# Optimization experiments

Hardware: AMD Instinct MI355X
Metric: run time of the kernel (lower is better)

## Reference

```python
import jax, jax.numpy as jnp
import numpy as np

B = 16384      # batch of protein embeddings
C = 128        # n_channels
F = 5000       # number of GO terms (functions)
E_CHILD = 15000  # parent->child edges (~3 children per term)


def setup_inputs() -> dict:
    key = jax.random.key(0)
    k_x, k_w, k_p, k_c = jax.random.split(key, 4)
    x = jax.random.normal(k_x, (B, C), dtype=jnp.float32)
    W = jax.random.normal(k_w, (C, F), dtype=jnp.float32) * 0.05
    b = jnp.zeros((F,), dtype=jnp.float32)
    # random GO DAG edges; every node also gets a self-edge so the max
    # aggregation covers {self} U children, exactly like the torch loop
    parents = jax.random.randint(k_p, (E_CHILD,), 0, F, dtype=jnp.int32)
    childs = jax.random.randint(k_c, (E_CHILD,), 0, F, dtype=jnp.int32)
    self_idx = jnp.arange(F, dtype=jnp.int32)
    edge_parent = jnp.concatenate([self_idx, parents])  # [20000]
    edge_child = jnp.concatenate([self_idx, childs])    # [20000]
    return {"x": x, "W": W, "b": b,
            "edge_parent": edge_parent, "edge_child": edge_child}


def reference(x, W, b, edge_parent, edge_child):
    # Fused version of the 5000 separate Linear(C,1)+Sigmoid heads
    probs = jax.nn.sigmoid(x @ W + b)          # [B, F]
    # Hierarchical max over {self} U children via segment-max on edge list
    vals = probs.T[edge_child]                  # [E, B]
    agg = jax.ops.segment_max(vals, edge_parent, num_segments=F)  # [F, B]
    return agg.T                                # [B, F]
```

## Files before the change

kernel.cpp:

```cpp
#include <hip/hip_runtime.h>
#include <hip/hip_bf16.h>

#define BDIM 16384
#define CDIM 128
#define FDIM 5000
#define EDIM 20000
#define ELLW 16
#define MAXOVF 20000
#define NT4  10

typedef __attribute__((ext_vector_type(8))) short short8;
typedef __attribute__((ext_vector_type(4))) float f32x4;
typedef __attribute__((ext_vector_type(2))) float f32x2;
typedef __attribute__((ext_vector_type(2))) int i32x2;
typedef __attribute__((ext_vector_type(8))) unsigned short upk8;
typedef __attribute__((ext_vector_type(4))) unsigned short upk4;
typedef __attribute__((ext_vector_type(2))) unsigned int u32x2;

__device__ __forceinline__ unsigned short f2bf(float f) {
    unsigned int u = __builtin_bit_cast(unsigned int, f);
    u = (u + 0x7fffu + ((u >> 16) & 1u)) >> 16;
    return (unsigned short)u;
}
__device__ __forceinline__ float bf2f(unsigned short s) {
    unsigned int u = ((unsigned int)s) << 16;
    return __builtin_bit_cast(float, u);
}
__device__ __forceinline__ unsigned short q2bf(unsigned int w, int k) {
    float f = (float)((w >> (8 * k)) & 0xFFu);
    return (unsigned short)(__builtin_bit_cast(unsigned int, f) >> 16);
}
__device__ __forceinline__ upk8 umax8(upk8 a, upk8 b) {
#if __has_builtin(__builtin_elementwise_max)
    return __builtin_elementwise_max(a, b);
#else
    upk8 r;
    #pragma unroll
    for (int j = 0; j < 8; ++j) r[j] = a[j] > b[j] ? a[j] : b[j];
    return r;
#endif
}
__device__ __forceinline__ float fast_rcp(float x) {
#if __has_builtin(__builtin_amdgcn_rcpf)
    return __builtin_amdgcn_rcpf(x);
#else
    return 1.0f / x;
#endif
}
__device__ __forceinline__ void gll16(const unsigned short* g, unsigned short* l) {
    __builtin_amdgcn_global_load_lds(
        (const __attribute__((address_space(1))) void*)g,
        (__attribute__((address_space(3))) void*)l, 16, 0, 0);
}

__global__ __launch_bounds__(256) void prep1_kernel(
    const float* __restrict__ x, const float* __restrict__ W,
    unsigned short* __restrict__ xb, unsigned short* __restrict__ wt,
    unsigned short* __restrict__ ell, int* __restrict__ cur,
    int* __restrict__ ovf_cnt)
{
    __shared__ float lt[128][33];
    int bid = blockIdx.x, tid = threadIdx.x;
    if (bid < 1024) {
        size_t base = (size_t)bid * 2048 + (size_t)tid * 8;
        const f32x4* p = (const f32x4*)(x + base);
        f32x4 v0 = p[0], v1 = p[1];
        short8 o;
        o[0] = (short)f2bf(v0[0]); o[1] = (short)f2bf(v0[1]);
        o[2] = (short)f2bf(v0[2]); o[3] = (short)f2bf(v0[3]);
        o[4] = (short)f2bf(v1[0]); o[5] = (short)f2bf(v1[1]);
        o[6] = (short)f2bf(v1[2]); o[7] = (short)f2bf(v1[3]);
        *(short8*)(xb + base) = o;
    } else if (bid < 1181) {
        int f0 = (bid - 1024) * 32;
        int f_l = tid & 31, k0 = (tid >> 5) * 16;
        #pragma unroll
        for (int i = 0; i < 16; ++i) {
            int f = f0 + f_l;
            lt[k0 + i][f_l] = (f < FDIM) ? W[(size_t)(k0 + i) * FDIM + f] : 0.f;
        }
        __syncthreads();
        int f_l2 = tid >> 3, ks = (tid & 7) * 16;
        int f = f0 + f_l2;
        if (f < FDIM) {
            short8 o0, o1;
            #pragma unroll
            for (int j = 0; j < 8; ++j) o0[j] = (short)f2bf(lt[ks + j][f_l2]);
            #pragma unroll
            for (int j = 0; j < 8; ++j) o1[j] = (short)f2bf(lt[ks + 8 + j][f_l2]);
            *(short8*)(wt + (size_t)f * 128 + ks)     = o0;
            *(short8*)(wt + (size_t)f * 128 + ks + 8) = o1;
        }
    } else {
        int p = (bid - 1181) * 256 + tid;
        if (p < FDIM) {
            upk8 s;
            #pragma unroll
            for (int j = 0; j < 8; ++j) s[j] = (unsigned short)p;
            *(upk8*)(ell + (size_t)p * ELLW)     = s;
            *(upk8*)(ell + (size_t)p * ELLW + 8) = s;
            cur[p] = 1;
        }
        if (p == FDIM) *ovf_cnt = 0;
    }
}

__global__ __launch_bounds__(256) void prep2_kernel(
    const int* __restrict__ epar, const int* __restrict__ echild,
    int* __restrict__ cur, unsigned short* __restrict__ ell,
    int* __restrict__ ovf_cnt, int* __restrict__ ovf_pairs)
{
    int i = blockIdx.x * 256 + threadIdx.x;
    if (i < EDIM) {
        int p = epar[i], c = echild[i];
        if (p != c) {
            int pos = atomicAdd(&cur[p], 1);
            if (pos < ELLW) {
                ell[(size_t)p * ELLW + pos] = (unsigned short)c;
            } else {
                int j = atomicAdd(ovf_cnt, 1);
                if (j < MAXOVF) { ovf_pairs[2 * j] = p; ovf_pairs[2 * j + 1] = c; }
            }
        }
    }
}

__global__ __launch_bounds__(512, 4) void gemm8i4_kernel(
    const unsigned short* __restrict__ xb,
    const unsigned short* __restrict__ wt,
    const float* __restrict__ bias,
    unsigned char* __restrict__ probs8)
{
    __shared__ unsigned short lA[128 * 128];
    __shared__ unsigned short lB[128 * 128];

    int bid0 = blockIdx.x;
    int bid  = (bid0 & 7) * (128 * NT4 / 8) + (bid0 >> 3);
    int bm = bid / NT4, bq = bid % NT4;
    int tid = threadIdx.x;
    int lane = tid & 63, w = tid >> 6;
    int wm = w >> 2, wn = w & 3;
    int g = lane >> 4, lr = lane & 15;
    int lrow = lane >> 4;
    int lcol = (lane & 15) << 4;

    auto stageA = [&]() {
        #pragma unroll
        for (int it = 0; it < 4; ++it) {
            int ci = w * 4 + it;
            int row = ci * 4 + lrow;
            int sw = lcol ^ ((row & 7) << 4);
            gll16(xb + ((size_t)(bm * 128 + row) << 7) + (sw >> 1),
                  lA + ci * 512);
        }
    };
    auto stageB = [&](int bn) {
        #pragma unroll
        for (int it = 0; it < 4; ++it) {
            int ci = w * 4 + it;
            int row = ci * 4 + lrow;
            int sw = lcol ^ ((row & 7) << 4);
            gll16(wt + ((size_t)(bn * 128 + row) << 7) + (sw >> 1),
                  lB + ci * 512);
        }
    };
    auto compute = [&](f32x4 (&acc)[4][2]) {
        #pragma unroll
        for (int ks = 0; ks < 4; ++ks) {
            int cbk = ks * 64 + g * 16;
            short8 af[4], bf[2];
            #pragma unroll
            for (int mi = 0; mi < 4; ++mi) {
                int row = wm * 64 + mi * 16 + lr;
                af[mi] = *(const short8*)((const char*)lA + row * 256 + (cbk ^ ((row & 7) << 4)));
            }
            #pragma unroll
            for (int nj = 0; nj < 2; ++nj) {
                int row = wn * 32 + nj * 16 + lr;
                bf[nj] = *(const short8*)((const char*)lB + row * 256 + (cbk ^ ((row & 7) << 4)));
            }
            #pragma unroll
            for (int mi = 0; mi < 4; ++mi)
                #pragma unroll
                for (int nj = 0; nj < 2; ++nj)
                    acc[mi][nj] = __builtin_amdgcn_mfma_f32_16x16x32_bf16(
                        af[mi], bf[nj], acc[mi][nj], 0, 0, 0);
        }
    };
    auto epilogue = [&](int bn, f32x4 (&acc)[4][2]) {
        #pragma unroll
        for (int nj = 0; nj < 2; ++nj) {
            int f = bn * 128 + wn * 32 + nj * 16 + lr;
            bool ok = (f < FDIM);
            float bb = ok ? bias[f] : 0.f;
            #pragma unroll
            for (int mi = 0; mi < 4; ++mi) {
                unsigned int pk = 0;
                #pragma unroll
                for (int j = 0; j < 4; ++j) {
                    float z = acc[mi][nj][j] + bb;
                    float pr = fast_rcp(1.0f + __expf(-z));
                    unsigned int q = (unsigned int)(pr * 255.f + 0.5f);
                    pk |= q << (8 * j);
                }
                if (ok) {
                    int slab = bm * 16 + wm * 8 + mi * 2 + (g >> 1);
                    *(unsigned int*)(probs8 + ((size_t)slab * FDIM + f) * 8 + (g & 1) * 4) = pk;
                }
            }
        }
    };

    stageA();
    stageB(bq * 4);
    __syncthreads();

    f32x4 zero = {0.f, 0.f, 0.f, 0.f};
    for (int t = 0; t < 4; ++t) {
        f32x4 acc[4][2];
        #pragma unroll
        for (int mi = 0; mi < 4; ++mi) { acc[mi][0] = zero; acc[mi][1] = zero; }
        compute(acc);
        if (t < 3) {
            __syncthreads();
            stageB(bq * 4 + t + 1);
            epilogue(bq * 4 + t, acc);
            __syncthreads();
        } else {
            epilogue(bq * 4 + t, acc);
        }
    }
}

__global__ __launch_bounds__(1024) void segmax10_kernel(
    const unsigned char* __restrict__ probs8,
    const int* __restrict__ cur, const unsigned short* __restrict__ ell,
    const int* __restrict__ ovf_cnt, const int* __restrict__ ovf_pairs,
    float* __restrict__ out)
{
    __shared__ unsigned short l[FDIM * 8];
    int slab = blockIdx.x;
    int b0 = slab * 8;
    int tid = threadIdx.x;
    const unsigned char* src = probs8 + (size_t)slab * FDIM * 8;

    for (int c = tid; c < FDIM; c += 1024) {
        u32x2 v = *(const u32x2*)(src + (size_t)c * 8);
        upk8 o;
        #pragma unroll
        for (int k = 0; k < 4; ++k) {
            o[k]     = q2bf(v[0], k);
            o[4 + k] = q2bf(v[1], k);
        }
        *(upk8*)(l + (size_t)c * 8) = o;
    }
    __syncthreads();

    int novf = *ovf_cnt; if (novf > MAXOVF) novf = MAXOVF;

    for (int p0 = tid * 2; p0 < FDIM; p0 += 2048) {
        int p1 = p0 + 1;
        i32x2 dg = *(const i32x2*)(cur + p0);
        upk4 ea = *(const upk4*)(ell + (size_t)p0 * ELLW);
        upk4 eb = *(const upk4*)(ell + (size_t)p1 * ELLW);
        upk8 ma = *(const upk8*)(l + (size_t)ea[0] * 8);
        upk8 mb = *(const upk8*)(l + (size_t)eb[0] * 8);
        ma = umax8(ma, *(const upk8*)(l + (size_t)ea[1] * 8));
        mb = umax8(mb, *(const upk8*)(l + (size_t)eb[1] * 8));
        ma = umax8(ma, *(const upk8*)(l + (size_t)ea[2] * 8));
        mb = umax8(mb, *(const upk8*)(l + (size_t)eb[2] * 8));
        ma = umax8(ma, *(const upk8*)(l + (size_t)ea[3] * 8));
        mb = umax8(mb, *(const upk8*)(l + (size_t)eb[3] * 8));
        if (dg[0] > 4) {
            upk4 e = *(const upk4*)(ell + (size_t)p0 * ELLW + 4);
            ma = umax8(ma, *(const upk8*)(l + (size_t)e[0] * 8));
            ma = umax8(ma, *(const upk8*)(l + (size_t)e[1] * 8));
            ma = umax8(ma, *(const upk8*)(l + (size_t)e[2] * 8));
            ma = umax8(ma, *(const upk8*)(l + (size_t)e[3] * 8));
        }
        if (dg[1] > 4) {
            upk4 e = *(const upk4*)(ell + (size_t)p1 * ELLW + 4);
            mb = umax8(mb, *(const upk8*)(l + (size_t)e[0] * 8));
            mb = umax8(mb, *(const upk8*)(l + (size_t)e[1] * 8));
            mb = umax8(mb, *(const upk8*)(l + (size_t)e[2] * 8));
            mb = umax8(mb, *(const upk8*)(l + (size_t)e[3] * 8));
        }
        if (dg[0] > 8) {
            upk8 e = *(const upk8*)(ell + (size_t)p0 * ELLW + 8);
            #pragma unroll
            for (int j = 0; j < 8; ++j)
                ma = umax8(ma, *(const upk8*)(l + (size_t)e[j] * 8));
        }
        if (dg[1] > 8) {
            upk8 e = *(const upk8*)(ell + (size_t)p1 * ELLW + 8);
            #pragma unroll
            for (int j = 0; j < 8; ++j)
                mb = umax8(mb, *(const upk8*)(l + (size_t)e[j] * 8));
        }
        if (dg[0] > ELLW) {
            for (int i = 0; i < novf; ++i)
                if (ovf_pairs[2 * i] == p0)
                    ma = umax8(ma, *(const upk8*)(l + (size_t)ovf_pairs[2 * i + 1] * 8));
        }
        if (dg[1] > ELLW) {
            for (int i = 0; i < novf; ++i)
                if (ovf_pairs[2 * i] == p1)
                    mb = umax8(mb, *(const upk8*)(l + (size_t)ovf_pairs[2 * i + 1] * 8));
        }
        size_t o = (size_t)b0 * FDIM + p0;
        #pragma unroll
        for (int r = 0; r < 8; ++r) {
            f32x2 v2;
            v2[0] = bf2f(ma[r]) * (1.f / 255.f);
            v2[1] = bf2f(mb[r]) * (1.f / 255.f);
            __builtin_nontemporal_store(v2, (f32x2*)(out + o + (size_t)r * FDIM));
        }
    }
}

extern "C" void kernel_launch(void* const* d_in, const int* in_sizes, int n_in,
                              void* d_out, int out_size, void* d_ws, size_t ws_size,
                              hipStream_t stream)
{
    const float* x     = (const float*)d_in[0];
    const float* W     = (const float*)d_in[1];
    const float* bias  = (const float*)d_in[2];
    const int*   epar  = (const int*)d_in[3];
    const int*   echild= (const int*)d_in[4];
    float* out = (float*)d_out;

    char* ws = (char*)d_ws;
    size_t off = 0;
    auto alloc = [&](size_t bytes) { size_t o = off; off = (off + bytes + 255) & ~(size_t)255; return o; };
    size_t o_probs  = alloc((size_t)BDIM * FDIM);
    size_t o_xb     = alloc((size_t)BDIM * CDIM * 2);
    size_t o_wt     = alloc((size_t)FDIM * CDIM * 2);
    size_t o_ell    = alloc((size_t)FDIM * ELLW * 2);
    size_t o_cur    = alloc((size_t)FDIM * 4);
    size_t o_ovfc   = alloc(4);
    size_t o_ovfp   = alloc((size_t)MAXOVF * 8);
    (void)ws_size; (void)in_sizes; (void)n_in; (void)out_size;

    unsigned char*  probs8 = (unsigned char*)(ws + o_probs);
    unsigned short* xb     = (unsigned short*)(ws + o_xb);
    unsigned short* wt     = (unsigned short*)(ws + o_wt);
    unsigned short* ell    = (unsigned short*)(ws + o_ell);
    int* cur      = (int*)(ws + o_cur);
    int* ovf_cnt  = (int*)(ws + o_ovfc);
    int* ovf_pairs= (int*)(ws + o_ovfp);

    prep1_kernel<<<1201, 256, 0, stream>>>(x, W, xb, wt, ell, cur, ovf_cnt);
    prep2_kernel<<<79, 256, 0, stream>>>(epar, echild, cur, ell, ovf_cnt, ovf_pairs);
    gemm8i4_kernel<<<128 * NT4, 512, 0, stream>>>(xb, wt, bias, probs8);
    segmax10_kernel<<<BDIM / 8, 1024, 0, stream>>>(probs8, cur, ell,
                                                   ovf_cnt, ovf_pairs, out);
}
```

Before: 159.2 us.

## Fuse GEMM and segment-max into persistent kernel with dynamic task queue

Result: slower. 220.6 us (+38.5%).

```diff
diff --git a/kernel.cpp b/kernel.cpp
--- a/kernel.cpp
+++ b/kernel.cpp
@@ -8,6 +8,10 @@
 #define ELLW 16
 #define MAXOVF 20000
 #define NT4  10
+#define NGEMM 1280
+#define NSEG  2048
+#define NBM   128
+#define LAGB  52
 
 typedef __attribute__((ext_vector_type(8))) short short8;
 typedef __attribute__((ext_vector_type(4))) float f32x4;
@@ -57,7 +61,8 @@
     const float* __restrict__ x, const float* __restrict__ W,
     unsigned short* __restrict__ xb, unsigned short* __restrict__ wt,
     unsigned short* __restrict__ ell, int* __restrict__ cur,
-    int* __restrict__ ovf_cnt)
+    int* __restrict__ ovf_cnt, int* __restrict__ task_ctr,
+    int* __restrict__ bm_done)
 {
     __shared__ float lt[128][33];
     int bid = blockIdx.x, tid = threadIdx.x;
@@ -101,7 +106,8 @@
             *(upk8*)(ell + (size_t)p * ELLW + 8) = s;
             cur[p] = 1;
         }
-        if (p == FDIM) *ovf_cnt = 0;
+        if (p < NBM) bm_done[p] = 0;
+        if (p == FDIM) { *ovf_cnt = 0; *task_ctr = 0; }
     }
 }
 
@@ -125,196 +131,229 @@
     }
 }
 
-__global__ __launch_bounds__(512, 4) void gemm8i4_kernel(
+__global__ __launch_bounds__(512, 4) void fused_kernel(
     const unsigned short* __restrict__ xb,
     const unsigned short* __restrict__ wt,
     const float* __restrict__ bias,
-    unsigned char* __restrict__ probs8)
+    unsigned char* __restrict__ probs8,
+    const int* __restrict__ cur, const unsigned short* __restrict__ ell,
+    const int* __restrict__ ovf_cnt, const int* __restrict__ ovf_pairs,
+    float* __restrict__ out,
+    int* __restrict__ task_ctr, int* __restrict__ bm_done)
 {
-    __shared__ unsigned short lA[128 * 128];
-    __shared__ unsigned short lB[128 * 128];
-
-    int bid0 = blockIdx.x;
-    int bid  = (bid0 & 7) * (128 * NT4 / 8) + (bid0 >> 3);
-    int bm = bid / NT4, bq = bid % NT4;
+    __shared__ unsigned short smem[40000];
+    __shared__ int sTask;
+
     int tid = threadIdx.x;
     int lane = tid & 63, w = tid >> 6;
     int wm = w >> 2, wn = w & 3;
     int g = lane >> 4, lr = lane & 15;
     int lrow = lane >> 4;
     int lcol = (lane & 15) << 4;
-
-    auto stageA = [&]() {
-        #pragma unroll
-        for (int it = 0; it < 4; ++it) {
-            int ci = w * 4 + it;
-            int row = ci * 4 + lrow;
-            int sw = lcol ^ ((row & 7) << 4);
-            gll16(xb + ((size_t)(bm * 128 + row) << 7) + (sw >> 1),
-                  lA + ci * 512);
-        }
-    };
-    auto stageB = [&](int bn) {
-        #pragma unroll
-        for (int it = 0; it < 4; ++it) {
-            int ci = w * 4 + it;
-            int row = ci * 4 + lrow;
-            int sw = lcol ^ ((row & 7) << 4);
-            gll16(wt + ((size_t)(bn * 128 + row) << 7) + (sw >> 1),
-                  lB + ci * 512);
-        }
-    };
-    auto compute = [&](f32x4 (&acc)[4][2]) {
-        #pragma unroll
-        for (int ks = 0; ks < 4; ++ks) {
-            int cbk = ks * 64 + g * 16;
-            short8 af[4], bf[2];
-            #pragma unroll
-            for (int mi = 0; mi < 4; ++mi) {
-                int row = wm * 64 + mi * 16 + lr;
-                af[mi] = *(const short8*)((const char*)lA + row * 256 + (cbk ^ ((row & 7) << 4)));
-            }
-            #pragma unroll
-            for (int nj = 0; nj < 2; ++nj) {
-                int row = wn * 32 + nj * 16 + lr;
-                bf[nj] = *(const short8*)((const char*)lB + row * 256 + (cbk ^ ((row & 7) << 4)));
-            }
-            #pragma unroll
-            for (int mi = 0; mi < 4; ++mi)
-                #pragma unroll
-                for (int nj = 0; nj < 2; ++nj)
-                    acc[mi][nj] = __builtin_amdgcn_mfma_f32_16x16x32_bf16(
-                        af[mi], bf[nj], acc[mi][nj], 0, 0, 0);
-        }
-    };
-    auto epilogue = [&](int bn, f32x4 (&acc)[4][2]) {
-        #pragma unroll
-        for (int nj = 0; nj < 2; ++nj) {
-            int f = bn * 128 + wn * 32 + nj * 16 + lr;
-            bool ok = (f < FDIM);
-            float bb = ok ? bias[f] : 0.f;
-            #pragma unroll
-            for (int mi = 0; mi < 4; ++mi) {
-                unsigned int pk = 0;
-                #pragma unroll
-                for (int j = 0; j < 4; ++j) {
-                    float z = acc[mi][nj][j] + bb;
-                    float pr = fast_rcp(1.0f + __expf(-z));
-                    unsigned int q = (unsigned int)(pr * 255.f + 0.5f);
-                    pk |= q << (8 * j);
-                }
-                if (ok) {
-                    int slab = bm * 16 + wm * 8 + mi * 2 + (g >> 1);
-                    *(unsigned int*)(probs8 + ((size_t)slab * FDIM + f) * 8 + (g & 1) * 4) = pk;
-                }
-            }
-        }
-    };
-
-    stageA();
-    stageB(bq * 4);
-    __syncthreads();
-
-    f32x4 zero = {0.f, 0.f, 0.f, 0.f};
-    for (int t = 0; t < 4; ++t) {
-        f32x4 acc[4][2];
-        #pragma unroll
-        for (int mi = 0; mi < 4; ++mi) { acc[mi][0] = zero; acc[mi][1] = zero; }
-        compute(acc);
-        if (t < 3) {
+    unsigned short* lA = smem;
+    unsigned short* lB = smem + 16384;
+
+    for (;;) {
+        if (tid == 0) sTask = atomicAdd(task_ctr, 1);
+        __syncthreads();
+        int task = sTask;
+        if (task >= NGEMM + NSEG) return;
+
+        int kind, bm = 0, bq = 0, slab = 0;
+        if (task < LAGB * 10) {
+            kind = 0; bm = task / 10; bq = task % 10;
+        } else {
+            int r = task - LAGB * 10;
+            if (r < (NBM - LAGB) * 26) {
+                int grp = r / 26, q = r % 26;
+                if (q < 10) { kind = 0; bm = LAGB + grp; bq = q; }
+                else        { kind = 1; slab = grp * 16 + (q - 10); }
+            } else {
+                kind = 1;
+                slab = (NBM - LAGB) * 16 + (r - (NBM - LAGB) * 26);
+            }
+        }
+
+        if (kind == 0) {
+            auto stageA = [&]() {
+                #pragma unroll
+                for (int it = 0; it < 4; ++it) {
+                    int ci = w * 4 + it;
+                    int row = ci * 4 + lrow;
+                    int sw = lcol ^ ((row & 7) << 4);
+                    gll16(xb + ((size_t)(bm * 128 + row) << 7) + (sw >> 1),
+                          lA + ci * 512);
+                }
+            };
+            auto stageB = [&](int bn) {
+                #pragma unroll
+                for (int it = 0; it < 4; ++it) {
+                    int ci = w * 4 + it;
+                    int row = ci * 4 + lrow;
+                    int sw = lcol ^ ((row & 7) << 4);
+                    gll16(wt + ((size_t)(bn * 128 + row) << 7) + (sw >> 1),
+                          lB + ci * 512);
+                }
+            };
+            auto compute = [&](f32x4 (&acc)[4][2]) {
+                #pragma unroll
+                for (int ks = 0; ks < 4; ++ks) {
+                    int cbk = ks * 64 + g * 16;
+                    short8 af[4], bf[2];
+                    #pragma unroll
+                    for (int mi = 0; mi < 4; ++mi) {
+                        int row = wm * 64 + mi * 16 + lr;
+                        af[mi] = *(const short8*)((const char*)lA + row * 256 + (cbk ^ ((row & 7) << 4)));
+                    }
+                    #pragma unroll
+                    for (int nj = 0; nj < 2; ++nj) {
+                        int row = wn * 32 + nj * 16 + lr;
+                        bf[nj] = *(const short8*)((const char*)lB + row * 256 + (cbk ^ ((row & 7) << 4)));
+                    }
+                    #pragma unroll
+                    for (int mi = 0; mi < 4; ++mi)
+                        #pragma unroll
+                        for (int nj = 0; nj < 2; ++nj)
+                            acc[mi][nj] = __builtin_amdgcn_mfma_f32_16x16x32_bf16(
+                                af[mi], bf[nj], acc[mi][nj], 0, 0, 0);
+                }
+            };
+            auto epilogue = [&](int bn, f32x4 (&acc)[4][2]) {
+                #pragma unroll
+                for (int nj = 0; nj < 2; ++nj) {
+                    int f = bn * 128 + wn * 32 + nj * 16 + lr;
+                    bool ok = (f < FDIM);
+                    float bb = ok ? bias[f] : 0.f;
+                    #pragma unroll
+                    for (int mi = 0; mi < 4; ++mi) {
+                        unsigned int pk = 0;
+                        #pragma unroll
+                        for (int j = 0; j < 4; ++j) {
+                            float z = acc[mi][nj][j] + bb;
+                            float pr = fast_rcp(1.0f + __expf(-z));
+                            unsigned int q = (unsigned int)(pr * 255.f + 0.5f);
+                            pk |= q << (8 * j);
+                        }
+                        if (ok) {
+                            int slb = bm * 16 + wm * 8 + mi * 2 + (g >> 1);
+                            *(unsigned int*)(probs8 + ((size_t)slb * FDIM + f) * 8 + (g & 1) * 4) = pk;
+                        }
+                    }
+                }
+            };
+
+            stageA();
+            stageB(bq * 4);
             __syncthreads();
-            stageB(bq * 4 + t + 1);
-            epilogue(bq * 4 + t, acc);
+
+            f32x4 zero = {0.f, 0.f, 0.f, 0.f};
+            for (int t = 0; t < 4; ++t) {
+                f32x4 acc[4][2];
+                #pragma unroll
+                for (int mi = 0; mi < 4; ++mi) { acc[mi][0] = zero; acc[mi][1] = zero; }
+                compute(acc);
+                if (t < 3) {
+                    __syncthreads();
+                    stageB(bq * 4 + t + 1);
+                    epilogue(bq * 4 + t, acc);
+                    __syncthreads();
+                } else {
+                    epilogue(bq * 4 + t, acc);
+                }
+            }
+
             __syncthreads();
+            if (tid == 0) {
+                __threadfence();
+                atomicAdd(&bm_done[bm], 1);
+            }
         } else {
-            epilogue(bq * 4 + t, acc);
-        }
-    }
-}
-
-__global__ __launch_bounds__(1024) void segmax10_kernel(
-    const unsigned char* __restrict__ probs8,
-    const int* __restrict__ cur, const unsigned short* __restrict__ ell,
-    const int* __restrict__ ovf_cnt, const int* __restrict__ ovf_pairs,
-    float* __restrict__ out)
-{
-    __shared__ unsigned short l[FDIM * 8];
-    int slab = blockIdx.x;
-    int b0 = slab * 8;
-    int tid = threadIdx.x;
-    const unsigned char* src = probs8 + (size_t)slab * FDIM * 8;
-
-    for (int c = tid; c < FDIM; c += 1024) {
-        u32x2 v = *(const u32x2*)(src + (size_t)c * 8);
-        upk8 o;
-        #pragma unroll
-        for (int k = 0; k < 4; ++k) {
-            o[k]     = q2bf(v[0], k);
-            o[4 + k] = q2bf(v[1], k);
-        }
-        *(upk8*)(l + (size_t)c * 8) = o;
-    }
-    __syncthreads();
-
-    int novf = *ovf_cnt; if (novf > MAXOVF) novf = MAXOVF;
-
-    for (int p0 = tid * 2; p0 < FDIM; p0 += 2048) {
-        int p1 = p0 + 1;
-        i32x2 dg = *(const i32x2*)(cur + p0);
-        upk4 ea = *(const upk4*)(ell + (size_t)p0 * ELLW);
-        upk4 eb = *(const upk4*)(ell + (size_t)p1 * ELLW);
-        upk8 ma = *(const upk8*)(l + (size_t)ea[0] * 8);
-        upk8 mb = *(const upk8*)(l + (size_t)eb[0] * 8);
-        ma = umax8(ma, *(const upk8*)(l + (size_t)ea[1] * 8));
-        mb = umax8(mb, *(const upk8*)(l + (size_t)eb[1] * 8));
-        ma = umax8(ma, *(const upk8*)(l + (size_t)ea[2] * 8));
-        mb = umax8(mb, *(const upk8*)(l + (size_t)eb[2] * 8));
-        ma = umax8(ma, *(const upk8*)(l + (size_t)ea[3] * 8));
-        mb = umax8(mb, *(const upk8*)(l + (size_t)eb[3] * 8));
-        if (dg[0] > 4) {
-            upk4 e = *(const upk4*)(ell + (size_t)p0 * ELLW + 4);
-            ma = umax8(ma, *(const upk8*)(l + (size_t)e[0] * 8));
-            ma = umax8(ma, *(const upk8*)(l + (size_t)e[1] * 8));
-            ma = umax8(ma, *(const upk8*)(l + (size_t)e[2] * 8));
-            ma = umax8(ma, *(const upk8*)(l + (size_t)e[3] * 8));
-        }
-        if (dg[1] > 4) {
-            upk4 e = *(const upk4*)(ell + (size_t)p1 * ELLW + 4);
-            mb = umax8(mb, *(const upk8*)(l + (size_t)e[0] * 8));
-            mb = umax8(mb, *(const upk8*)(l + (size_t)e[1] * 8));
-            mb = umax8(mb, *(const upk8*)(l + (size_t)e[2] * 8));
-            mb = umax8(mb, *(const upk8*)(l + (size_t)e[3] * 8));
-        }
-        if (dg[0] > 8) {
-            upk8 e = *(const upk8*)(ell + (size_t)p0 * ELLW + 8);
-            #pragma unroll
-            for (int j = 0; j < 8; ++j)
-                ma = umax8(ma, *(const upk8*)(l + (size_t)e[j] * 8));
-        }
-        if (dg[1] > 8) {
-            upk8 e = *(const upk8*)(ell + (size_t)p1 * ELLW + 8);
-            #pragma unroll
-            for (int j = 0; j < 8; ++j)
-                mb = umax8(mb, *(const upk8*)(l + (size_t)e[j] * 8));
-        }
-        if (dg[0] > ELLW) {
-            for (int i = 0; i < novf; ++i)
-                if (ovf_pairs[2 * i] == p0)
-                    ma = umax8(ma, *(const upk8*)(l + (size_t)ovf_pairs[2 * i + 1] * 8));
-        }
-        if (dg[1] > ELLW) {
-            for (int i = 0; i < novf; ++i)
-                if (ovf_pairs[2 * i] == p1)
-                    mb = umax8(mb, *(const upk8*)(l + (size_t)ovf_pairs[2 * i + 1] * 8));
-        }
-        size_t o = (size_t)b0 * FDIM + p0;
-        #pragma unroll
-        for (int r = 0; r < 8; ++r) {
-            f32x2 v2;
-            v2[0] = bf2f(ma[r]) * (1.f / 255.f);
-            v2[1] = bf2f(mb[r]) * (1.f / 255.f);
-            __builtin_nontemporal_store(v2, (f32x2*)(out + o + (size_t)r * FDIM));
-        }
+            int sbm = slab >> 4;
+            if (tid == 0) {
+                while (atomicAdd(&bm_done[sbm], 0) < NT4)
+                    __builtin_amdgcn_s_sleep(8);
+            }
+            __syncthreads();
+            asm volatile("" ::: "memory");
+
+            unsigned short* l = smem;
+            int b0 = slab * 8;
+            const unsigned char* src = probs8 + (size_t)slab * FDIM * 8;
+
+            for (int c = tid; c < FDIM; c += 512) {
+                u32x2 v = *(const u32x2*)(src + (size_t)c * 8);
+                upk8 o;
+                #pragma unroll
+                for (int k = 0; k < 4; ++k) {
+                    o[k]     = q2bf(v[0], k);
+                    o[4 + k] = q2bf(v[1], k);
+                }
+                *(upk8*)(l + (size_t)c * 8) = o;
+            }
+            __syncthreads();
+
+            int novf = *ovf_cnt; if (novf > MAXOVF) novf = MAXOVF;
+
+            for (int p0 = tid * 2; p0 < FDIM; p0 += 1024) {
+                int p1 = p0 + 1;
+                i32x2 dg = *(const i32x2*)(cur + p0);
+                upk4 ea = *(const upk4*)(ell + (size_t)p0 * ELLW);
+                upk4 eb = *(const upk4*)(ell + (size_t)p1 * ELLW);
+                upk8 ma = *(const upk8*)(l + (size_t)ea[0] * 8);
+                upk8 mb = *(const upk8*)(l + (size_t)eb[0] * 8);
+                ma = umax8(ma, *(const upk8*)(l + (size_t)ea[1] * 8));
+                mb = umax8(mb, *(const upk8*)(l + (size_t)eb[1] * 8));
+                ma = umax8(ma, *(const upk8*)(l + (size_t)ea[2] * 8));
+                mb = umax8(mb, *(const upk8*)(l + (size_t)eb[2] * 8));
+                ma = umax8(ma, *(const upk8*)(l + (size_t)ea[3] * 8));
+                mb = umax8(mb, *(const upk8*)(l + (size_t)eb[3] * 8));
+                if (dg[0] > 4) {
+                    upk4 e = *(const upk4*)(ell + (size_t)p0 * ELLW + 4);
+                    ma = umax8(ma, *(const upk8*)(l + (size_t)e[0] * 8));
+                    ma = umax8(ma, *(const upk8*)(l + (size_t)e[1] * 8));
+                    ma = umax8(ma, *(const upk8*)(l + (size_t)e[2] * 8));
+                    ma = umax8(ma, *(const upk8*)(l + (size_t)e[3] * 8));
+                }
+                if (dg[1] > 4) {
+                    upk4 e = *(const upk4*)(ell + (size_t)p1 * ELLW + 4);
+                    mb = umax8(mb, *(const upk8*)(l + (size_t)e[0] * 8));
+                    mb = umax8(mb, *(const upk8*)(l + (size_t)e[1] * 8));
+                    mb = umax8(mb, *(const upk8*)(l + (size_t)e[2] * 8));
+                    mb = umax8(mb, *(const upk8*)(l + (size_t)e[3] * 8));
+                }
+                if (dg[0] > 8) {
+                    upk8 e = *(const upk8*)(ell + (size_t)p0 * ELLW + 8);
+                    #pragma unroll
+                    for (int j = 0; j < 8; ++j)
+                        ma = umax8(ma, *(const upk8*)(l + (size_t)e[j] * 8));
+                }
+                if (dg[1] > 8) {
+                    upk8 e = *(const upk8*)(ell + (size_t)p1 * ELLW + 8);
+                    #pragma unroll
+                    for (int j = 0; j < 8; ++j)
+                        mb = umax8(mb, *(const upk8*)(l + (size_t)e[j] * 8));
+                }
+                if (dg[0] > ELLW) {
+                    for (int i = 0; i < novf; ++i)
+                        if (ovf_pairs[2 * i] == p0)
+                            ma = umax8(ma, *(const upk8*)(l + (size_t)ovf_pairs[2 * i + 1] * 8));
+                }
+                if (dg[1] > ELLW) {
+                    for (int i = 0; i < novf; ++i)
+                        if (ovf_pairs[2 * i] == p1)
+                            mb = umax8(mb, *(const upk8*)(l + (size_t)ovf_pairs[2 * i + 1] * 8));
+                }
+                size_t o = (size_t)b0 * FDIM + p0;
+                #pragma unroll
+                for (int r = 0; r < 8; ++r) {
+                    f32x2 v2;
+                    v2[0] = bf2f(ma[r]) * (1.f / 255.f);
+                    v2[1] = bf2f(mb[r]) * (1.f / 255.f);
+                    __builtin_nontemporal_store(v2, (f32x2*)(out + o + (size_t)r * FDIM));
+                }
+            }
+        }
+        __syncthreads();
     }
 }
 
@@ -339,6 +378,8 @@
     size_t o_cur    = alloc((size_t)FDIM * 4);
     size_t o_ovfc   = alloc(4);
     size_t o_ovfp   = alloc((size_t)MAXOVF * 8);
+    size_t o_tc     = alloc(4);
+    size_t o_bmd    = alloc((size_t)NBM * 4);
     (void)ws_size; (void)in_sizes; (void)n_in; (void)out_size;
 
     unsigned char*  probs8 = (unsigned char*)(ws + o_probs);
@@ -348,10 +389,13 @@
     int* cur      = (int*)(ws + o_cur);
     int* ovf_cnt  = (int*)(ws + o_ovfc);
     int* ovf_pairs= (int*)(ws + o_ovfp);
-
-    prep1_kernel<<<1201, 256, 0, stream>>>(x, W, xb, wt, ell, cur, ovf_cnt);
+    int* task_ctr = (int*)(ws + o_tc);
+    int* bm_done  = (int*)(ws + o_bmd);
+
+    prep1_kernel<<<1201, 256, 0, stream>>>(x, W, xb, wt, ell, cur, ovf_cnt,
+                                           task_ctr, bm_done);
     prep2_kernel<<<79, 256, 0, stream>>>(epar, echild, cur, ell, ovf_cnt, ovf_pairs);
-    gemm8i4_kernel<<<128 * NT4, 512, 0, stream>>>(xb, wt, bias, probs8);
-    segmax10_kernel<<<BDIM / 8, 1024, 0, stream>>>(probs8, cur, ell,
-                                                   ovf_cnt, ovf_pairs, out);
-}
+    fused_kernel<<<512, 512, 0, stream>>>(xb, wt, bias, probs8, cur, ell,
+                                          ovf_cnt, ovf_pairs, out,
+                                          task_ctr, bm_done);
+}
```

## Defer sigmoid past max using order-preserving bf16 keys for logits

Applied to the files above, without the earlier changes.

After: 153.8 us. 1.04x faster.

```diff
diff --git a/kernel.cpp b/kernel.cpp
--- a/kernel.cpp
+++ b/kernel.cpp
@@ -25,10 +25,6 @@
 __device__ __forceinline__ float bf2f(unsigned short s) {
     unsigned int u = ((unsigned int)s) << 16;
     return __builtin_bit_cast(float, u);
-}
-__device__ __forceinline__ unsigned short q2bf(unsigned int w, int k) {
-    float f = (float)((w >> (8 * k)) & 0xFFu);
-    return (unsigned short)(__builtin_bit_cast(unsigned int, f) >> 16);
 }
 __device__ __forceinline__ upk8 umax8(upk8 a, upk8 b) {
 #if __has_builtin(__builtin_elementwise_max)
@@ -46,6 +42,14 @@
 #else
     return 1.0f / x;
 #endif
+}
+__device__ __forceinline__ unsigned int key2(unsigned int h) {
+    unsigned int t = (h >> 15) & 0x00010001u;
+    return h ^ (t * 0x7FFFu + 0x80008000u);
+}
+__device__ __forceinline__ unsigned short unkey(unsigned short k) {
+    unsigned int s = (k >> 15) & 1u;
+    return (unsigned short)(k ^ (0x8000u + ((s ^ 1u) * 0x7FFFu)));
 }
 __device__ __forceinline__ void gll16(const unsigned short* g, unsigned short* l) {
     __builtin_amdgcn_global_load_lds(
@@ -125,11 +129,11 @@
     }
 }
 
-__global__ __launch_bounds__(512, 4) void gemm8i4_kernel(
+__global__ __launch_bounds__(512, 4) void gemm8k_kernel(
     const unsigned short* __restrict__ xb,
     const unsigned short* __restrict__ wt,
     const float* __restrict__ bias,
-    unsigned char* __restrict__ probs8)
+    unsigned short* __restrict__ probs16)
 {
     __shared__ unsigned short lA[128 * 128];
     __shared__ unsigned short lB[128 * 128];
@@ -195,17 +199,19 @@
             float bb = ok ? bias[f] : 0.f;
             #pragma unroll
             for (int mi = 0; mi < 4; ++mi) {
-                unsigned int pk = 0;
-                #pragma unroll
-                for (int j = 0; j < 4; ++j) {
-                    float z = acc[mi][nj][j] + bb;
-                    float pr = fast_rcp(1.0f + __expf(-z));
-                    unsigned int q = (unsigned int)(pr * 255.f + 0.5f);
-                    pk |= q << (8 * j);
-                }
+                float z0 = acc[mi][nj][0] + bb;
+                float z1 = acc[mi][nj][1] + bb;
+                float z2 = acc[mi][nj][2] + bb;
+                float z3 = acc[mi][nj][3] + bb;
+                unsigned int h01, h23;
+                asm("v_cvt_pk_bf16_f32 %0, %1, %2" : "=v"(h01) : "v"(z0), "v"(z1));
+                asm("v_cvt_pk_bf16_f32 %0, %1, %2" : "=v"(h23) : "v"(z2), "v"(z3));
+                u32x2 st;
+                st[0] = key2(h01);
+                st[1] = key2(h23);
                 if (ok) {
                     int slab = bm * 16 + wm * 8 + mi * 2 + (g >> 1);
-                    *(unsigned int*)(probs8 + ((size_t)slab * FDIM + f) * 8 + (g & 1) * 4) = pk;
+                    *(u32x2*)(probs16 + ((size_t)slab * FDIM + f) * 8 + (g & 1) * 4) = st;
                 }
             }
         }
@@ -232,8 +238,8 @@
     }
 }
 
-__global__ __launch_bounds__(1024) void segmax10_kernel(
-    const unsigned char* __restrict__ probs8,
+__global__ __launch_bounds__(1024) void segmax12_kernel(
+    const unsigned short* __restrict__ probs16,
     const int* __restrict__ cur, const unsigned short* __restrict__ ell,
     const int* __restrict__ ovf_cnt, const int* __restrict__ ovf_pairs,
     float* __restrict__ out)
@@ -242,17 +248,10 @@
     int slab = blockIdx.x;
     int b0 = slab * 8;
     int tid = threadIdx.x;
-    const unsigned char* src = probs8 + (size_t)slab * FDIM * 8;
+    const unsigned short* src = probs16 + (size_t)slab * FDIM * 8;
 
     for (int c = tid; c < FDIM; c += 1024) {
-        u32x2 v = *(const u32x2*)(src + (size_t)c * 8);
-        upk8 o;
-        #pragma unroll
-        for (int k = 0; k < 4; ++k) {
-            o[k]     = q2bf(v[0], k);
-            o[4 + k] = q2bf(v[1], k);
-        }
-        *(upk8*)(l + (size_t)c * 8) = o;
+        gll16(src + (size_t)c * 8, l + (size_t)c * 8);
     }
     __syncthreads();
 
@@ -310,9 +309,11 @@
         size_t o = (size_t)b0 * FDIM + p0;
         #pragma unroll
         for (int r = 0; r < 8; ++r) {
+            float za = bf2f(unkey(ma[r]));
+            float zb = bf2f(unkey(mb[r]));
             f32x2 v2;
-            v2[0] = bf2f(ma[r]) * (1.f / 255.f);
-            v2[1] = bf2f(mb[r]) * (1.f / 255.f);
+            v2[0] = fast_rcp(1.0f + __expf(-za));
+            v2[1] = fast_rcp(1.0f + __expf(-zb));
             __builtin_nontemporal_store(v2, (f32x2*)(out + o + (size_t)r * FDIM));
         }
     }
@@ -332,7 +333,7 @@
     char* ws = (char*)d_ws;
     size_t off = 0;
     auto alloc = [&](size_t bytes) { size_t o = off; off = (off + bytes + 255) & ~(size_t)255; return o; };
-    size_t o_probs  = alloc((size_t)BDIM * FDIM);
+    size_t o_probs  = alloc((size_t)BDIM * FDIM * 2);
     size_t o_xb     = alloc((size_t)BDIM * CDIM * 2);
     size_t o_wt     = alloc((size_t)FDIM * CDIM * 2);
     size_t o_ell    = alloc((size_t)FDIM * ELLW * 2);
@@ -341,17 +342,17 @@
     size_t o_ovfp   = alloc((size_t)MAXOVF * 8);
     (void)ws_size; (void)in_sizes; (void)n_in; (void)out_size;
 
-    unsigned char*  probs8 = (unsigned char*)(ws + o_probs);
-    unsigned short* xb     = (unsigned short*)(ws + o_xb);
-    unsigned short* wt     = (unsigned short*)(ws + o_wt);
-    unsigned short* ell    = (unsigned short*)(ws + o_ell);
+    unsigned short* probs16 = (unsigned short*)(ws + o_probs);
+    unsigned short* xb      = (unsigned short*)(ws + o_xb);
+    unsigned short* wt      = (unsigned short*)(ws + o_wt);
+    unsigned short* ell     = (unsigned short*)(ws + o_ell);
     int* cur      = (int*)(ws + o_cur);
     int* ovf_cnt  = (int*)(ws + o_ovfc);
     int* ovf_pairs= (int*)(ws + o_ovfp);
 
     prep1_kernel<<<1201, 256, 0, stream>>>(x, W, xb, wt, ell, cur, ovf_cnt);
     prep2_kernel<<<79, 256, 0, stream>>>(epar, echild, cur, ell, ovf_cnt, ovf_pairs);
-    gemm8i4_kernel<<<128 * NT4, 512, 0, stream>>>(xb, wt, bias, probs8);
-    segmax10_kernel<<<BDIM / 8, 1024, 0, stream>>>(probs8, cur, ell,
+    gemm8k_kernel<<<128 * NT4, 512, 0, stream>>>(xb, wt, bias, probs16);
+    segmax12_kernel<<<BDIM / 8, 1024, 0, stream>>>(probs16, cur, ell,
                                                    ovf_cnt, ovf_pairs, out);
 }
```
